# Kernel tuning notes

Hardware: AMD Instinct MI355X
Metric: run time of the kernel (lower is better)

The kernel has to match this reference:

```python
import jax, jax.numpy as jnp
import numpy as np

N_COARSE = 100_000
M_FINE = 4 * N_COARSE
GRID = 128
C_IN, C_HID, C_OUT = 32, 64, 32
K3 = 27   # 3x3x3 neighborhood
K2 = 8    # 2x2x2 transposed-conv offsets


def setup_inputs() -> dict:
    rng = np.random.default_rng(0)
    # --- sparse coarse grid: N unique voxels in GRID^3 ---
    lin = np.sort(rng.choice(GRID ** 3, size=N_COARSE, replace=False))
    cx, cy, cz = lin // (GRID * GRID), (lin // GRID) % GRID, lin % GRID
    coords = np.stack([cx, cy, cz], 1).astype(np.int64)
    # --- rulebook: neighbor index per voxel per 3^3 offset (sentinel = N) ---
    offs = np.array([(dx, dy, dz) for dx in (-1, 0, 1) for dy in (-1, 0, 1) for dz in (-1, 0, 1)])
    nbr = np.full((N_COARSE, K3), N_COARSE, np.int32)
    for k in range(K3):
        nc = coords + offs[k]
        valid = ((nc >= 0) & (nc < GRID)).all(1)
        nlin = nc[:, 0] * GRID * GRID + nc[:, 1] * GRID + nc[:, 2]
        pos = np.clip(np.searchsorted(lin, nlin), 0, N_COARSE - 1)
        found = valid & (lin[pos] == nlin)
        nbr[found, k] = pos[found].astype(np.int32)
    # --- fine grid: 4 distinct children (of 8) per coarse voxel ---
    child = np.argsort(rng.random((N_COARSE, K2)), axis=1)[:, :4].astype(np.int32)
    parent_idx = np.repeat(np.arange(N_COARSE, dtype=np.int32), 4)
    offset_idx = child.reshape(-1)

    key = jax.random.key(0)
    ks = jax.random.split(key, 16)
    nrm = lambda k, sh, fan: (jax.random.normal(k, sh, jnp.float32) / np.sqrt(fan)).astype(jnp.float32)
    return {
        "feats_in": jax.random.normal(ks[0], (N_COARSE, C_IN), jnp.float32),
        "x_up_feats": jax.random.normal(ks[1], (M_FINE, C_OUT), jnp.float32),
        "nbr_idx": jnp.asarray(nbr),
        "parent_idx": jnp.asarray(parent_idx),
        "offset_idx": jnp.asarray(offset_idx),
        "W_enc1": nrm(ks[2], (K3, C_IN, C_HID), K3 * C_IN),
        "b_enc1": jnp.zeros((C_HID,), jnp.float32),
        "W_enc2": nrm(ks[3], (K3, C_HID, C_HID), K3 * C_HID),
        "b_enc2": jnp.zeros((C_HID,), jnp.float32),
        "W_enc3": nrm(ks[4], (K3, C_HID, C_HID), K3 * C_HID),
        "b_enc3": jnp.zeros((C_HID,), jnp.float32),
        "W_t": nrm(ks[5], (K2, C_HID, C_HID), C_HID),
        "b_t": jnp.zeros((C_HID,), jnp.float32),
        "W_d1": nrm(ks[6], (C_HID, C_HID), C_HID),
        "b_d1": jnp.zeros((C_HID,), jnp.float32),
        "W_d2": nrm(ks[7], (C_HID, C_OUT), C_HID),
        "b_d2": jnp.zeros((C_OUT,), jnp.float32),
    }


def _sparse_conv3(x, nbr, W, b):
    """3x3x3 stride-1 sparse conv: gather neighbors, per-offset matmul, accumulate.
    x: [N,Cin], nbr: [N,27] (sentinel N -> zero feature), W: [27,Cin,Cout]."""
    xp = jnp.concatenate([x, jnp.zeros((1, x.shape[1]), x.dtype)], 0)  # sentinel row
    acc = jnp.broadcast_to(b, (x.shape[0], W.shape[-1]))
    for k in range(W.shape[0]):  # fixed 27-way structural loop
        acc = acc + xp[nbr[:, k]] @ W[k]
    return acc


def _t_conv2(x, parent_idx, offset_idx, W, b):
    """2x2x2 stride-2 transposed sparse conv onto a given fine grid.
    x: [N,C], parent_idx: [M] (sentinel N), offset_idx: [M] in [0,8)."""
    xp = jnp.concatenate([x, jnp.zeros((1, x.shape[1]), x.dtype)], 0)
    g = xp[parent_idx]  # [M,C]
    out = jnp.broadcast_to(b, (g.shape[0], W.shape[-1]))
    for k in range(W.shape[0]):  # fixed 8-way structural loop
        out = out + jnp.where((offset_idx == k)[:, None], g @ W[k], 0.0)
    return out


def reference(feats_in, x_up_feats, nbr_idx, parent_idx, offset_idx,
              W_enc1, b_enc1, W_enc2, b_enc2, W_enc3, b_enc3,
              W_t, b_t, W_d1, b_d1, W_d2, b_d2):
    # encoder: (conv -> dropout[eval: identity] -> relu) x 3
    x = jax.nn.relu(_sparse_conv3(feats_in, nbr_idx, W_enc1, b_enc1))
    x = jax.nn.relu(_sparse_conv3(x, nbr_idx, W_enc2, b_enc2))
    x = jax.nn.relu(_sparse_conv3(x, nbr_idx, W_enc3, b_enc3))
    # transposed upsample conv onto x_upsample's grid
    x = _t_conv2(x, parent_idx, offset_idx, W_t, b_t)
    # decoder: relu -> 1x1 conv -> relu -> 1x1 conv, then residual add
    x = jax.nn.relu(x) @ W_d1 + b_d1
    x = jax.nn.relu(x) @ W_d2 + b_d2
    return x + x_up_feats
```

## Files before the change

kernel.cpp:

```cpp
#include <hip/hip_runtime.h>
#include <hip/hip_bf16.h>

#define NC 100000
#define MF 400000
#define K3 27

typedef __bf16 bf16_t;
typedef bf16_t bf16x8 __attribute__((ext_vector_type(8)));
typedef float  f32x4  __attribute__((ext_vector_type(4)));

#define O_E1 0
#define O_E2 55296
#define O_E3 165888
#define O_T  276480
#define O_D1 309248
#define O_D2 313344
#define W_TOTAL 315392

__device__ __align__(16) bf16_t g_w[W_TOTAL];
__device__ __align__(16) bf16_t g_x0[(size_t)NC * 32];
__device__ __align__(16) bf16_t g_x1[(size_t)NC * 64];
__device__ __align__(16) bf16_t g_x2[(size_t)NC * 64];
__device__ int g_nbrT[(size_t)K3 * NC];

static __device__ __forceinline__ bf16x8 zero8() {
    bf16x8 v;
#pragma unroll
    for (int i = 0; i < 8; ++i) v[i] = (bf16_t)0.0f;
    return v;
}

__global__ __launch_bounds__(256) void prep_k(
    const float* __restrict__ W_e1, const float* __restrict__ W_e2,
    const float* __restrict__ W_e3, const float* __restrict__ W_t,
    const float* __restrict__ W_d1, const float* __restrict__ W_d2,
    const float* __restrict__ feats, const int* __restrict__ nbr)
{
    int b = blockIdx.x;
    if (b < 154) {
        int tid = b * 256 + threadIdx.x;
        int lane = tid & 63;
        int f = tid >> 6;
        const float* src; int doff, nt, nc, fb;
        if      (f < 108) { src = W_e1; doff = O_E1; nt = 4; nc = 1; fb = 0;   }
        else if (f < 324) { src = W_e2; doff = O_E2; nt = 4; nc = 2; fb = 108; }
        else if (f < 540) { src = W_e3; doff = O_E3; nt = 4; nc = 2; fb = 324; }
        else if (f < 604) { src = W_t;  doff = O_T;  nt = 4; nc = 2; fb = 540; }
        else if (f < 612) { src = W_d1; doff = O_D1; nt = 4; nc = 2; fb = 604; }
        else              { src = W_d2; doff = O_D2; nt = 2; nc = 2; fb = 612; }
        int lf = f - fb;
        int t  = lf % nt;
        int c  = (lf / nt) % nc;
        int ko = lf / (nt * nc);
        int Cin = nc * 32, Cout = nt * 16;
        int n  = t * 16 + (lane & 15);
        int kb = c * 32 + (lane >> 4) * 8;
        bf16x8 tmp;
#pragma unroll
        for (int j = 0; j < 8; ++j)
            tmp[j] = (bf16_t)src[((size_t)ko * Cin + (kb + j)) * Cout + n];
        *(bf16x8*)(g_w + doff + (size_t)lf * 512 + lane * 8) = tmp;
    } else if (b < 1717) {
        int i = (b - 154) * 256 + threadIdx.x;
        if (i < NC * 32 / 8) {
            const f32x4* p = (const f32x4*)(feats + (size_t)i * 8);
            f32x4 lo = p[0], hi = p[1];
            bf16x8 v;
#pragma unroll
            for (int j = 0; j < 4; ++j) { v[j] = (bf16_t)lo[j]; v[j + 4] = (bf16_t)hi[j]; }
            *(bf16x8*)(g_x0 + (size_t)i * 8) = v;
        }
    } else {
        int r = (b - 1717) * 256 + threadIdx.x;
        if (r < NC) {
#pragma unroll
            for (int k = 0; k < K3; ++k)
                g_nbrT[(size_t)k * NC + r] = nbr[(size_t)r * K3 + k];
        }
    }
}

#define TS 72

#define STAGE_B(KO, P) do {                                                    \
    _Pragma("unroll")                                                          \
    for (int i_ = 0; i_ < CH * 2; ++i_) {                                      \
        const bf16_t* gs_ = wsrc + (size_t)(KO) * CH * 2048                    \
                          + wv * (CH * 1024) + i_ * 512 + lane * 8;            \
        __builtin_amdgcn_global_load_lds(                                      \
            (const __attribute__((address_space(1))) void*)gs_,                \
            (__attribute__((address_space(3))) void*)                          \
                (&bB[P][wv * (CH * 1024) + i_ * 512 + lane * 8]),              \
            16, 0, 0);                                                         \
    }                                                                          \
} while (0)

#define GATHER_A(P) do {                                                       \
    _Pragma("unroll")                                                          \
    for (int c_ = 0; c_ < CH; ++c_)                                            \
        _Pragma("unroll")                                                      \
        for (int mt_ = 0; mt_ < 2; ++mt_) {                                    \
            int ii_ = idxbuf[P][mt_];                                          \
            bool va_ = (unsigned)ii_ < (unsigned)NC;                           \
            int ss_ = va_ ? ii_ : 0;                                           \
            bf16x8 a_ = *(const bf16x8*)(xb + (size_t)ss_ * CIN + c_ * 32 + q * 8); \
            if (!va_) a_ = zero8();                                            \
            abuf[P][c_][mt_] = a_;                                             \
        }                                                                      \
} while (0)

#define LOAD_IDX(KO, P) do {                                                   \
    _Pragma("unroll")                                                          \
    for (int mt_ = 0; mt_ < 2; ++mt_) {                                        \
        int r_ = base + mt_ * 16 + cl;                                         \
        idxbuf[P][mt_] = (r_ < NC) ? g_nbrT[(size_t)(KO) * NC + r_] : NC;      \
    }                                                                          \
} while (0)

#define MFMA_KO(P) do {                                                        \
    _Pragma("unroll")                                                          \
    for (int c_ = 0; c_ < CH; ++c_) {                                          \
        bf16x8 bfr_[4];                                                        \
        _Pragma("unroll")                                                      \
        for (int t_ = 0; t_ < 4; ++t_)                                         \
            bfr_[t_] = *(const bf16x8*)&bB[P][(c_ * 4 + t_) * 512 + lane * 8]; \
        _Pragma("unroll")                                                      \
        for (int mt_ = 0; mt_ < 2; ++mt_)                                      \
            _Pragma("unroll")                                                  \
            for (int t_ = 0; t_ < 4; ++t_)                                     \
                acc[mt_][t_] = __builtin_amdgcn_mfma_f32_16x16x32_bf16(        \
                    abuf[P][c_][mt_], bfr_[t_], acc[mt_][t_], 0, 0, 0);        \
    }                                                                          \
} while (0)

#define CSTEP_FULL(KO, P) do {                                                 \
    STAGE_B((KO) + 1, (P) ^ 1);                                                \
    __builtin_amdgcn_sched_barrier(0);         \
    GATHER_A((P) ^ 1);                                                         \
    LOAD_IDX((KO) + 2, P);                                                     \
    MFMA_KO(P);                                                                \
    asm volatile("s_waitcnt vmcnt(%0)\n\ts_barrier"                            \
                 :: "i"(CH * 2 + 2) : "memory");                               \
    __builtin_amdgcn_sched_barrier(0);                     \
} while (0)

#define CSTEP_PEN(KO, P) do {                \
    STAGE_B((KO) + 1, (P) ^ 1);                                                \
    __builtin_amdgcn_sched_barrier(0);                                         \
    GATHER_A((P) ^ 1);                                                         \
    MFMA_KO(P);                                                                \
    asm volatile("s_waitcnt vmcnt(%0)\n\ts_barrier"                            \
                 :: "i"(CH * 2) : "memory");                                   \
    __builtin_amdgcn_sched_barrier(0);                                         \
} while (0)

template <int CH>
__global__ __launch_bounds__(128, 2) void conv_k(
    int w_off,
    const float* __restrict__ bias,
    int src_sel, int dst_sel)
{
    constexpr int CIN = CH * 32;
    const bf16_t* xb = (src_sel == 0) ? g_x0 : (src_sel == 1 ? g_x1 : g_x2);
    bf16_t* y = (dst_sel == 1) ? g_x1 : g_x2;
    const bf16_t* wsrc = g_w + w_off;

    __shared__ __align__(16) bf16_t bB[2][4096];
    int tid = threadIdx.x;
    int wv = tid >> 6, lane = tid & 63;
    int cl = lane & 15, q = lane >> 4;

    int per = gridDim.x >> 3;
    int blk = (blockIdx.x & 7) * per + (blockIdx.x >> 3);
    int base = blk * 64 + wv * 32;

    int idxbuf[2][2];
    bf16x8 abuf[2][CH][2];

    LOAD_IDX(0, 0);
    GATHER_A(0);
    LOAD_IDX(1, 1);
    STAGE_B(0, 0);

    f32x4 acc[2][4];
#pragma unroll
    for (int t = 0; t < 4; ++t) {
        float b = bias[t * 16 + cl];
#pragma unroll
        for (int mt = 0; mt < 2; ++mt) acc[mt][t] = (f32x4){b, b, b, b};
    }
    __syncthreads();

    for (int ko = 0; ko < 24; ko += 2) {
        CSTEP_FULL(ko, 0);
        CSTEP_FULL(ko + 1, 1);
    }
    CSTEP_FULL(24, 0);
    CSTEP_PEN(25, 1);
    MFMA_KO(0);
    __syncthreads();

    bf16_t* tb = ((bf16_t*)bB) + wv * 2304;
#pragma unroll
    for (int mt2 = 0; mt2 < 2; ++mt2)
#pragma unroll
        for (int t = 0; t < 4; ++t)
#pragma unroll
            for (int r = 0; r < 4; ++r) {
                float v = acc[mt2][t][r];
                v = v > 0.0f ? v : 0.0f;
                tb[(mt2 * 16 + q * 4 + r) * TS + t * 16 + cl] = (bf16_t)v;
            }
#pragma unroll
    for (int i = 0; i < 4; ++i) {
        int rl = i * 8 + (lane >> 3);
        int c8 = (lane & 7) * 8;
        bf16x8 v8 = *(const bf16x8*)&tb[rl * TS + c8];
        int orow = base + rl;
        if (orow < NC)
            *(bf16x8*)(y + (size_t)orow * 64 + c8) = v8;
    }
}

#define HS 72
__global__ __launch_bounds__(128) void tconv_dec_k(
    const int*   __restrict__ offs,
    const float* __restrict__ b_t,
    const float* __restrict__ b_d1,
    const float* __restrict__ b_d2,
    const float* __restrict__ x_up,
    float*       __restrict__ out)
{
    __shared__ __align__(16) bf16_t h_lds[2][64 * HS];
    __shared__ __align__(16) int off_lds[2][64];
    int wv = threadIdx.x >> 6, lane = threadIdx.x & 63;
    int cl = lane & 15, q = lane >> 4;
    int per = gridDim.x >> 3;
    int blk = (blockIdx.x & 7) * per + (blockIdx.x >> 3);
    int p0 = (blk * 2 + wv) * 16;
    int fbase = p0 * 4;

    {
        int fi = fbase + lane;
        off_lds[wv][lane] = (fi < MF) ? offs[fi] : 0;
    }
    int code[4];
#pragma unroll
    for (int r = 0; r < 4; ++r) {
        int4 o = *(const int4*)&off_lds[wv][(q * 4 + r) * 4];
        code[r] = (1 << (4 * o.x)) | (2 << (4 * o.y)) |
                  (3 << (4 * o.z)) | (4 << (4 * o.w));
    }

    bool pv = (p0 + cl) < NC;
    size_t xrow = (size_t)(pv ? p0 + cl : 0) * 64;
    bf16x8 ax[2];
#pragma unroll
    for (int c = 0; c < 2; ++c) {
        bf16x8 t8 = *(const bf16x8*)(g_x1 + xrow + c * 32 + q * 8);
        ax[c] = pv ? t8 : zero8();
    }

    const bf16_t* wt = g_w + O_T;
#pragma unroll
    for (int k = 0; k < 8; ++k) {
        f32x4 acc[4];
#pragma unroll
        for (int t = 0; t < 4; ++t) {
            float b = b_t[t * 16 + cl];
            acc[t] = (f32x4){b, b, b, b};
        }
#pragma unroll
        for (int c = 0; c < 2; ++c) {
            const bf16_t* wb = wt + ((size_t)(k * 2 + c) * 4) * 512 + lane * 8;
#pragma unroll
            for (int t = 0; t < 4; ++t) {
                bf16x8 b = *(const bf16x8*)(wb + t * 512);
                acc[t] = __builtin_amdgcn_mfma_f32_16x16x32_bf16(ax[c], b, acc[t], 0, 0, 0);
            }
        }
#pragma unroll
        for (int r = 0; r < 4; ++r) {
            int nib = (code[r] >> (4 * k)) & 0xF;
            if (nib) {
                int fl = (((q * 4 + r) * 4) + (nib - 1)) & 63;
#pragma unroll
                for (int t = 0; t < 4; ++t) {
                    float v = acc[t][r];
                    v = v > 0.0f ? v : 0.0f;
                    h_lds[wv][fl * HS + t * 16 + cl] = (bf16_t)v;
                }
            }
        }
    }

    bf16x8 a1[4][2];
#pragma unroll
    for (int mt = 0; mt < 4; ++mt)
#pragma unroll
        for (int c = 0; c < 2; ++c)
            a1[mt][c] = *(const bf16x8*)&h_lds[wv][(mt * 16 + cl) * HS + c * 32 + q * 8];

#pragma unroll
    for (int mt = 0; mt < 4; ++mt) {
        f32x4 acc2[4];
#pragma unroll
        for (int t = 0; t < 4; ++t) {
            float b = b_d1[t * 16 + cl];
            acc2[t] = (f32x4){b, b, b, b};
        }
#pragma unroll
        for (int c = 0; c < 2; ++c)
#pragma unroll
            for (int t = 0; t < 4; ++t) {
                bf16x8 b = *(const bf16x8*)(g_w + O_D1 + (size_t)(c * 4 + t) * 512 + lane * 8);
                acc2[t] = __builtin_amdgcn_mfma_f32_16x16x32_bf16(a1[mt][c], b, acc2[t], 0, 0, 0);
            }
#pragma unroll
        for (int t = 0; t < 4; ++t)
#pragma unroll
            for (int r = 0; r < 4; ++r) {
                float v = acc2[t][r];
                v = v > 0.0f ? v : 0.0f;
                h_lds[wv][(mt * 16 + q * 4 + r) * HS + t * 16 + cl] = (bf16_t)v;
            }
    }

    float* fW = (float*)h_lds[wv];
#pragma unroll
    for (int mt = 0; mt < 4; ++mt) {
        bf16x8 a2[2];
#pragma unroll
        for (int c = 0; c < 2; ++c)
            a2[c] = *(const bf16x8*)&h_lds[wv][(mt * 16 + cl) * HS + c * 32 + q * 8];
        f32x4 acc3[2];
#pragma unroll
        for (int t = 0; t < 2; ++t) {
            float b = b_d2[t * 16 + cl];
            acc3[t] = (f32x4){b, b, b, b};
        }
#pragma unroll
        for (int c = 0; c < 2; ++c)
#pragma unroll
            for (int t = 0; t < 2; ++t) {
                bf16x8 b = *(const bf16x8*)(g_w + O_D2 + (size_t)(c * 2 + t) * 512 + lane * 8);
                acc3[t] = __builtin_amdgcn_mfma_f32_16x16x32_bf16(a2[c], b, acc3[t], 0, 0, 0);
            }
#pragma unroll
        for (int t = 0; t < 2; ++t)
#pragma unroll
            for (int r = 0; r < 4; ++r)
                fW[(mt * 16 + q * 4 + r) * 36 + t * 16 + cl] = acc3[t][r];
    }

#pragma unroll
    for (int i = 0; i < 8; ++i) {
        int rl = i * 8 + (lane >> 3);
        int c4 = (lane & 7) * 4;
        int fg = fbase + rl;
        if (fg < MF) {
            f32x4 xv = *(const f32x4*)(x_up + (size_t)fg * 32 + c4);
            f32x4 v = *(const f32x4*)&fW[rl * 36 + c4];
            v += xv;
            *(f32x4*)(out + (size_t)fg * 32 + c4) = v;
        }
    }
}

extern "C" void kernel_launch(void* const* d_in, const int* in_sizes, int n_in,
                              void* d_out, int out_size, void* d_ws, size_t ws_size,
                              hipStream_t stream) {
    const float* feats  = (const float*)d_in[0];
    const float* x_up   = (const float*)d_in[1];
    const int*   nbr    = (const int*)d_in[2];
    const int*   offs   = (const int*)d_in[4];
    const float* W_e1 = (const float*)d_in[5];
    const float* b_e1 = (const float*)d_in[6];
    const float* W_e2 = (const float*)d_in[7];
    const float* b_e2 = (const float*)d_in[8];
    const float* W_e3 = (const float*)d_in[9];
    const float* b_e3 = (const float*)d_in[10];
    const float* W_t  = (const float*)d_in[11];
    const float* b_t  = (const float*)d_in[12];
    const float* W_d1 = (const float*)d_in[13];
    const float* b_d1 = (const float*)d_in[14];
    const float* W_d2 = (const float*)d_in[15];
    const float* b_d2 = (const float*)d_in[16];
    float* out = (float*)d_out;

    prep_k<<<2108, 256, 0, stream>>>(W_e1, W_e2, W_e3, W_t, W_d1, W_d2, feats, nbr);

    conv_k<1><<<1568, 128, 0, stream>>>(O_E1, b_e1, 0, 1);
    conv_k<2><<<1568, 128, 0, stream>>>(O_E2, b_e2, 1, 2);
    conv_k<2><<<1568, 128, 0, stream>>>(O_E3, b_e3, 2, 1);

    tconv_dec_k<<<3128, 128, 0, stream>>>(offs, b_t, b_d1, b_d2, x_up, out);
}
```

Measured before the change: 285.1 us.

## Deepen sparse conv gather/weight pipeline from double to triple buffering

The 27-offset conv main loop now keeps three stages in flight instead of two. Neighbour gathers, weight staging into LDS and index loads are issued two offsets ahead of the MFMA work, with adjusted vmcnt wait counts and a hand-written drain at the end. The aim is to hide more gather latency behind the matrix multiplies. The cost is more LDS (three 8 KB buffers) and more VGPRs for the extra A-fragment buffer, which may reduce occupancy under the 128x2 launch bound.

```diff
diff --git a/kernel.cpp b/kernel.cpp
--- a/kernel.cpp
+++ b/kernel.cpp
@@ -133,25 +133,15 @@
     }                                                                          \
 } while (0)
 
-#define CSTEP_FULL(KO, P) do {                                                 \
-    STAGE_B((KO) + 1, (P) ^ 1);                                                \
-    __builtin_amdgcn_sched_barrier(0);         \
-    GATHER_A((P) ^ 1);                                                         \
-    LOAD_IDX((KO) + 2, P);                                                     \
+#define CSTEP3(KO, P, P2) do {                                                 \
+    STAGE_B((KO) + 2, P2);                                                     \
+    __builtin_amdgcn_sched_barrier(0);                \
+    GATHER_A(P2);                            \
+    LOAD_IDX((KO) + 3, P);                       \
     MFMA_KO(P);                                                                \
     asm volatile("s_waitcnt vmcnt(%0)\n\ts_barrier"                            \
-                 :: "i"(CH * 2 + 2) : "memory");                               \
+                 :: "i"(CH * 6 + 4) : "memory");                               \
     __builtin_amdgcn_sched_barrier(0);                     \
-} while (0)
-
-#define CSTEP_PEN(KO, P) do {                \
-    STAGE_B((KO) + 1, (P) ^ 1);                                                \
-    __builtin_amdgcn_sched_barrier(0);                                         \
-    GATHER_A((P) ^ 1);                                                         \
-    MFMA_KO(P);                                                                \
-    asm volatile("s_waitcnt vmcnt(%0)\n\ts_barrier"                            \
-                 :: "i"(CH * 2) : "memory");                                   \
-    __builtin_amdgcn_sched_barrier(0);                                         \
 } while (0)
 
 template <int CH>
@@ -165,7 +155,7 @@
     bf16_t* y = (dst_sel == 1) ? g_x1 : g_x2;
     const bf16_t* wsrc = g_w + w_off;
 
-    __shared__ __align__(16) bf16_t bB[2][4096];
+    __shared__ __align__(16) bf16_t bB[3][4096];
     int tid = threadIdx.x;
     int wv = tid >> 6, lane = tid & 63;
     int cl = lane & 15, q = lane >> 4;
@@ -174,13 +164,16 @@
     int blk = (blockIdx.x & 7) * per + (blockIdx.x >> 3);
     int base = blk * 64 + wv * 32;
 
-    int idxbuf[2][2];
-    bf16x8 abuf[2][CH][2];
+    int idxbuf[3][2];
+    bf16x8 abuf[3][CH][2];
 
     LOAD_IDX(0, 0);
+    LOAD_IDX(1, 1);
+    LOAD_IDX(2, 2);
     GATHER_A(0);
-    LOAD_IDX(1, 1);
+    GATHER_A(1);
     STAGE_B(0, 0);
+    STAGE_B(1, 1);
 
     f32x4 acc[2][4];
 #pragma unroll
@@ -191,13 +184,23 @@
     }
     __syncthreads();
 
-    for (int ko = 0; ko < 24; ko += 2) {
-        CSTEP_FULL(ko, 0);
-        CSTEP_FULL(ko + 1, 1);
-    }
-    CSTEP_FULL(24, 0);
-    CSTEP_PEN(25, 1);
+    for (int ko = 0; ko < 24; ko += 3) {
+        CSTEP3(ko,     0, 2);
+        CSTEP3(ko + 1, 1, 0);
+        CSTEP3(ko + 2, 2, 1);
+    }
+    STAGE_B(26, 2);
+    __builtin_amdgcn_sched_barrier(0);
+    GATHER_A(2);
     MFMA_KO(0);
+    asm volatile("s_waitcnt vmcnt(%0)\n\ts_barrier"
+                 :: "i"(CH * 6 + 2) : "memory");
+    __builtin_amdgcn_sched_barrier(0);
+    MFMA_KO(1);
+    asm volatile("s_waitcnt vmcnt(%0)\n\ts_barrier"
+                 :: "i"(CH * 2) : "memory");
+    __builtin_amdgcn_sched_barrier(0);
+    MFMA_KO(2);
     __syncthreads();
 
     bf16_t* tb = ((bf16_t*)bB) + wv * 2304;
```

Result: slower. 308.3 us (+8.1%).
